# Performance work log

Measured on AMD Instinct MI355X. Metric: run time of the kernel, lower is better.

Reference implementation:

```python
import jax, jax.numpy as jnp
import numpy as np

DIM = 768
HEADS = 12
HEAD_DIM = DIM // HEADS
SEQ = 196
BATCH = 64
SCALE = HEAD_DIM ** -0.5


def setup_inputs() -> dict:
    key = jax.random.key(0)
    ks = jax.random.split(key, 5)
    x = jax.random.normal(ks[0], (BATCH, SEQ, DIM), dtype=jnp.float32)
    W_qkv = jax.random.normal(ks[1], (DIM, 3 * DIM), dtype=jnp.float32) * (DIM ** -0.5)
    static_a = jax.random.truncated_normal(ks[2], -2.0, 2.0, (1, HEADS, SEQ, SEQ), dtype=jnp.float32)
    W_proj = jax.random.normal(ks[3], (DIM, DIM), dtype=jnp.float32) * (DIM ** -0.5)
    b_proj = jnp.zeros((DIM,), dtype=jnp.float32)
    return {"x": x, "W_qkv": W_qkv, "static_a": static_a, "W_proj": W_proj, "b_proj": b_proj}


def reference(x, W_qkv, static_a, W_proj, b_proj):
    B, N, C = x.shape
    qkv = (x @ W_qkv).reshape(B, N, 3, HEADS, HEAD_DIM)
    qkv = jnp.transpose(qkv, (2, 0, 3, 1, 4))  # [3, B, H, N, D]
    q, k, v = qkv[0], qkv[1], qkv[2]
    attn = jnp.einsum('bhnd,bhmd->bhnm', q, k) * SCALE
    attn = jax.nn.softmax(attn, axis=-1) + static_a  # post-softmax additive bias
    out = jnp.einsum('bhnm,bhmd->bhnd', attn, v)  # [B, H, N, D]
    out = jnp.transpose(out, (0, 2, 1, 3)).reshape(B, N, C)
    return out @ W_proj + b_proj
```

## Files before the change

### kernel.cpp

```cpp
#include <hip/hip_runtime.h>
#include <stdint.h>

#define DIM 768
#define HEADS 12
#define SEQ 196
#define BATCH 64
#define NTOK (BATCH*SEQ)
#define QKVLD (3*DIM)
#define SCALE 0.125f

using short8  = __attribute__((ext_vector_type(8))) short;
using short4v = __attribute__((ext_vector_type(4))) short;
using float4v = __attribute__((ext_vector_type(4))) float;
using ushort4v = __attribute__((ext_vector_type(4))) unsigned short;

static __device__ __forceinline__ unsigned short f2bf(float f) {
  union { float f; unsigned u; } v; v.f = f;
  unsigned u = v.u;
  u += 0x7fffu + ((u >> 16) & 1u);
  return (unsigned short)(u >> 16);
}

#if defined(__has_builtin)
#if __has_builtin(__builtin_amdgcn_global_load_lds)
#define HAS_GLL 1
#endif
#endif

static __device__ __forceinline__ void gll16(const unsigned short* g, unsigned short* l) {
#ifdef HAS_GLL
  __builtin_amdgcn_global_load_lds(
      (const __attribute__((address_space(1))) void*)g,
      (__attribute__((address_space(3))) void*)l, 16, 0, 0);
#else
  const int lane = threadIdx.x & 63;
  *(short8*)(l + lane * 8) = *(const short8*)g;
#endif
}

__global__ __launch_bounds__(256) void cast_x_kernel(const float* __restrict__ in,
                                                     unsigned short* __restrict__ out) {
  int i = blockIdx.x * 256 + threadIdx.x;
  float4 v = ((const float4*)in)[i];
  ushort4v o;
  o.x = f2bf(v.x); o.y = f2bf(v.y); o.z = f2bf(v.z); o.w = f2bf(v.w);
  ((ushort4v*)out)[i] = o;
}

__global__ __launch_bounds__(256) void transpose_cast_kernel(const float* __restrict__ in,
                                                             unsigned short* __restrict__ out,
                                                             int R, int C) {
  __shared__ float tile[32][33];
  int c0 = blockIdx.x * 32, r0 = blockIdx.y * 32;
  int tx = threadIdx.x, ty = threadIdx.y;
  for (int i = 0; i < 32; i += 8)
    tile[ty + i][tx] = in[(size_t)(r0 + ty + i) * C + c0 + tx];
  __syncthreads();
  for (int i = 0; i < 32; i += 8)
    out[(size_t)(c0 + ty + i) * R + r0 + tx] = f2bf(tile[tx][ty + i]);
}

template <int MODE>
__global__ __launch_bounds__(256) void gemm_kernel(const unsigned short* __restrict__ A,
                                                   const unsigned short* __restrict__ Bt,
                                                   const float* __restrict__ bias,
                                                   unsigned short* __restrict__ outB,
                                                   float* __restrict__ outF) {
  constexpr int K = 768;
  __shared__ __align__(16) unsigned short Als[2][128 * 32];
  __shared__ __align__(16) unsigned short Bls[2][128 * 32];
  const int tid = threadIdx.x;
  const int wid = tid >> 6, lane = tid & 63;
  const int s = lane & 15, q = lane >> 4;
  const int wr = wid >> 1, wc = wid & 1;
  const int m0 = blockIdx.y * 128;
  const int n0 = blockIdx.x * 128;

  float4v acc[4][4];
  for (int i = 0; i < 4; i++)
    for (int j = 0; j < 4; j++) acc[i][j] = (float4v){0.f, 0.f, 0.f, 0.f};

  const int srow = lane >> 2;
  const int scol = (lane & 3) * 8;

  const unsigned short* ga = A  + (size_t)(m0 + wid * 32 + srow) * K + scol;
  const unsigned short* gb = Bt + (size_t)(n0 + wid * 32 + srow) * K + scol;
  unsigned short* la0 = &Als[0][wid * 32 * 32];
  unsigned short* la1 = &Als[1][wid * 32 * 32];
  unsigned short* lb0 = &Bls[0][wid * 32 * 32];
  unsigned short* lb1 = &Bls[1][wid * 32 * 32];

  for (int kt = 0; kt < K; kt += 64) {
    gll16(ga,                la0);
    gll16(ga + 16 * K,       la0 + 16 * 32);
    gll16(ga + 32,           la1);
    gll16(ga + 32 + 16 * K,  la1 + 16 * 32);
    gll16(gb,                lb0);
    gll16(gb + 16 * K,       lb0 + 16 * 32);
    gll16(gb + 32,           lb1);
    gll16(gb + 32 + 16 * K,  lb1 + 16 * 32);
    ga += 64; gb += 64;
    __syncthreads();

    for (int hh = 0; hh < 2; hh++) {
      short8 af[4], bfr[4];
      for (int i = 0; i < 4; i++)
        af[i] = *(const short8*)&Als[hh][(wr * 64 + i * 16 + s) * 32 + q * 8];
      for (int j = 0; j < 4; j++)
        bfr[j] = *(const short8*)&Bls[hh][(wc * 64 + j * 16 + s) * 32 + q * 8];
      for (int i = 0; i < 4; i++)
        for (int j = 0; j < 4; j++)
          acc[i][j] = __builtin_amdgcn_mfma_f32_16x16x32_bf16(bfr[j], af[i], acc[i][j], 0, 0, 0);
    }
    __syncthreads();
  }

  if (MODE == 0) {
    for (int i = 0; i < 4; i++) {
      size_t mrow = (size_t)(m0 + wr * 64 + i * 16 + s) * QKVLD;
      for (int j = 0; j < 4; j++) {
        int n = n0 + wc * 64 + j * 16 + q * 4;
        ushort4v ov;
        ov.x = f2bf(acc[i][j][0]); ov.y = f2bf(acc[i][j][1]);
        ov.z = f2bf(acc[i][j][2]); ov.w = f2bf(acc[i][j][3]);
        *(ushort4v*)&outB[mrow + n] = ov;
      }
    }
  } else {
    for (int i = 0; i < 4; i++) {
      size_t mrow = (size_t)(m0 + wr * 64 + i * 16 + s) * 768;
      for (int j = 0; j < 4; j++) {
        int n = n0 + wc * 64 + j * 16 + q * 4;
        float4v bv = *(const float4v*)&bias[n];
        float4v o;
        for (int r = 0; r < 4; r++) o[r] = acc[i][j][r] + bv[r];
        *(float4v*)&outF[mrow + n] = o;
      }
    }
  }
}

__global__ __launch_bounds__(256) void attn_kernel(const unsigned short* __restrict__ qkv,
                                                   const float* __restrict__ static_a,
                                                   unsigned short* __restrict__ outA) {
  constexpr int WV = 228;
  __shared__ __align__(16) unsigned short Vt[64 * WV];
  const int tid = threadIdx.x, wid = tid >> 6, lane = tid & 63;
  const int s = lane & 15, q = lane >> 4;
  const int bh = blockIdx.x;
  const int b = bh / 12, h = bh % 12;
  const unsigned short* Qb = qkv + (size_t)b * SEQ * QKVLD + h * 64;
  const unsigned short* Kb = Qb + 768;
  const unsigned short* Vb = Qb + 1536;

  {
    const int ms = tid & 63;
    const int d0 = (tid >> 6) * 16;
    for (int mb = 0; mb < 4; ++mb) {
      int m = mb * 64 + ms;
      if (m < 224) {
        if (m < 196) {
          short8 v0 = *(const short8*)&Vb[(size_t)m * QKVLD + d0];
          short8 v1 = *(const short8*)&Vb[(size_t)m * QKVLD + d0 + 8];
          for (int j = 0; j < 8; j++) Vt[(d0 + j) * WV + m] = (unsigned short)v0[j];
          for (int j = 0; j < 8; j++) Vt[(d0 + 8 + j) * WV + m] = (unsigned short)v1[j];
        } else {
          for (int j = 0; j < 16; j++) Vt[(d0 + j) * WV + m] = 0;
        }
      }
    }
  }
  __syncthreads();

  const int pmbase = (s >> 2) * 8 + (s & 3);

  for (int qt = wid; qt < 13; qt += 4) {
    const int n0 = qt * 16;
    const int nq = n0 + s;
    const int nql = nq > 195 ? 195 : nq;
    short8 qf0 = *(const short8*)&Qb[(size_t)nql * QKVLD + q * 8];
    short8 qf1 = *(const short8*)&Qb[(size_t)nql * QKVLD + 32 + q * 8];

    float4v sacc[14];
    for (int tt = 0; tt < 13; tt++) {
      int t = tt >> 1, h4 = tt & 1;
      int m = t * 32 + h4 * 4 + pmbase;
      if (m > 195) m = 195;
      short8 kf0 = *(const short8*)&Kb[(size_t)m * QKVLD + q * 8];
      short8 kf1 = *(const short8*)&Kb[(size_t)m * QKVLD + 32 + q * 8];
      float4v z = (float4v){0.f, 0.f, 0.f, 0.f};
      z = __builtin_amdgcn_mfma_f32_16x16x32_bf16(kf0, qf0, z, 0, 0, 0);
      z = __builtin_amdgcn_mfma_f32_16x16x32_bf16(kf1, qf1, z, 0, 0, 0);
      sacc[tt] = z;
    }
    sacc[13] = (float4v){0.f, 0.f, 0.f, 0.f};

    float mx = -3.0e38f;
    for (int tt = 0; tt < 12; tt++)
      for (int i = 0; i < 4; i++) mx = fmaxf(mx, sacc[tt][i]);
    if (q == 0)
      for (int i = 0; i < 4; i++) mx = fmaxf(mx, sacc[12][i]);
    mx = fmaxf(mx, __shfl_xor(mx, 16));
    mx = fmaxf(mx, __shfl_xor(mx, 32));
    const float CE = SCALE * 1.44269504f;
    float sm = 0.f;
    for (int tt = 0; tt < 12; tt++)
      for (int i = 0; i < 4; i++) {
        float e = __builtin_amdgcn_exp2f((sacc[tt][i] - mx) * CE);
        sacc[tt][i] = e; sm += e;
      }
    if (q == 0) {
      for (int i = 0; i < 4; i++) {
        float e = __builtin_amdgcn_exp2f((sacc[12][i] - mx) * CE);
        sacc[12][i] = e; sm += e;
      }
    } else {
      sacc[12] = (float4v){0.f, 0.f, 0.f, 0.f};
    }
    sm += __shfl_xor(sm, 16);
    sm += __shfl_xor(sm, 32);
    const float inv = 1.0f / sm;

    const float* sa = static_a + ((size_t)h * SEQ + nql) * SEQ;
    short8 pfrag[7];
    for (int t = 0; t < 7; t++) {
      short8 pf;
      for (int h4 = 0; h4 < 2; h4++) {
        int tt = 2 * t + h4;
        bool valid = (tt < 12) || (tt == 12 && q == 0);
        float4v a4 = (float4v){0.f, 0.f, 0.f, 0.f};
        if (valid) a4 = *(const float4v*)(sa + t * 32 + q * 8 + h4 * 4);
        int src = valid ? tt : 13;
        for (int i = 0; i < 4; i++) {
          float pv = valid ? (sacc[src][i] * inv + a4[i]) : 0.f;
          pf[h4 * 4 + i] = (short)f2bf(pv);
        }
      }
      pfrag[t] = pf;
    }

    for (int dt = 0; dt < 4; dt++) {
      float4v o = (float4v){0.f, 0.f, 0.f, 0.f};
      for (int t = 0; t < 7; t++) {
        const unsigned short* vp = &Vt[(dt * 16 + s) * WV + t * 32 + q * 8];
        short4v v0 = *(const short4v*)vp;
        short4v v1 = *(const short4v*)(vp + 4);
        short8 vf;
        vf[0] = v0[0]; vf[1] = v0[1]; vf[2] = v0[2]; vf[3] = v0[3];
        vf[4] = v1[0]; vf[5] = v1[1]; vf[6] = v1[2]; vf[7] = v1[3];
        o = __builtin_amdgcn_mfma_f32_16x16x32_bf16(vf, pfrag[t], o, 0, 0, 0);
      }
      if (nq < 196) {
        ushort4v ov;
        ov.x = f2bf(o[0]); ov.y = f2bf(o[1]); ov.z = f2bf(o[2]); ov.w = f2bf(o[3]);
        *(ushort4v*)&outA[((size_t)b * SEQ + nq) * DIM + h * 64 + dt * 16 + q * 4] = ov;
      }
    }
  }
}

extern "C" void kernel_launch(void* const* d_in, const int* in_sizes, int n_in,
                              void* d_out, int out_size, void* d_ws, size_t ws_size,
                              hipStream_t stream) {
  const float* x        = (const float*)d_in[0];
  const float* Wqkv     = (const float*)d_in[1];
  const float* static_a = (const float*)d_in[2];
  const float* Wproj    = (const float*)d_in[3];
  const float* bproj    = (const float*)d_in[4];
  float* out = (float*)d_out;

  unsigned char* ws = (unsigned char*)d_ws;
  size_t off = 0;
  unsigned short* qkv_ws = (unsigned short*)(ws + off); off += (size_t)NTOK * QKVLD * 2;
  unsigned short* xa_ws  = (unsigned short*)(ws + off); off += (size_t)NTOK * DIM * 2;
  unsigned short* wqkvt  = (unsigned short*)(ws + off); off += (size_t)3 * DIM * DIM * 2;
  unsigned short* wprojt = (unsigned short*)(ws + off); off += (size_t)DIM * DIM * 2;

  cast_x_kernel<<<NTOK * DIM / 4 / 256, 256, 0, stream>>>(x, xa_ws);
  transpose_cast_kernel<<<dim3(3 * DIM / 32, DIM / 32), dim3(32, 8), 0, stream>>>(Wqkv, wqkvt, DIM, 3 * DIM);
  transpose_cast_kernel<<<dim3(DIM / 32, DIM / 32), dim3(32, 8), 0, stream>>>(Wproj, wprojt, DIM, DIM);
  gemm_kernel<0><<<dim3(3 * DIM / 128, NTOK / 128), 256, 0, stream>>>(xa_ws, wqkvt, nullptr, qkv_ws, nullptr);
  attn_kernel<<<BATCH * HEADS, 256, 0, stream>>>(qkv_ws, static_a, xa_ws);
  gemm_kernel<1><<<dim3(DIM / 128, NTOK / 128), 256, 0, stream>>>(xa_ws, wprojt, bproj, nullptr, out);
}
```

Measured before the change: 263.8 us.

## Replace LDS-staged GEMM with per-wave register-tiled direct global loads

Both GEMMs drop shared-memory staging and block-wide barriers. Each wave now computes its own 64x64 output tile, loading MFMA fragments straight from global memory into double-buffered registers, and the launch becomes a 1D grid with an occupancy hint. This removes LDS traffic and __syncthreads stalls, but the four waves in a block no longer share loaded A/B tiles, so global/L2 traffic per FLOP rises and the fragment loads are strided 16-byte reads.

Result: slower. 395.8 us (+50.0%).

```diff
diff --git a/kernel.cpp b/kernel.cpp
--- a/kernel.cpp
+++ b/kernel.cpp
@@ -19,23 +19,6 @@
   unsigned u = v.u;
   u += 0x7fffu + ((u >> 16) & 1u);
   return (unsigned short)(u >> 16);
-}
-
-#if defined(__has_builtin)
-#if __has_builtin(__builtin_amdgcn_global_load_lds)
-#define HAS_GLL 1
-#endif
-#endif
-
-static __device__ __forceinline__ void gll16(const unsigned short* g, unsigned short* l) {
-#ifdef HAS_GLL
-  __builtin_amdgcn_global_load_lds(
-      (const __attribute__((address_space(1))) void*)g,
-      (__attribute__((address_space(3))) void*)l, 16, 0, 0);
-#else
-  const int lane = threadIdx.x & 63;
-  *(short8*)(l + lane * 8) = *(const short8*)g;
-#endif
 }
 
 __global__ __launch_bounds__(256) void cast_x_kernel(const float* __restrict__ in,
@@ -61,65 +44,56 @@
 }
 
 template <int MODE>
-__global__ __launch_bounds__(256) void gemm_kernel(const unsigned short* __restrict__ A,
-                                                   const unsigned short* __restrict__ Bt,
-                                                   const float* __restrict__ bias,
-                                                   unsigned short* __restrict__ outB,
-                                                   float* __restrict__ outF) {
+__global__ __launch_bounds__(256, 3) void gemm_kernel(const unsigned short* __restrict__ A,
+                                                      const unsigned short* __restrict__ Bt,
+                                                      const float* __restrict__ bias,
+                                                      unsigned short* __restrict__ outB,
+                                                      float* __restrict__ outF) {
   constexpr int K = 768;
-  __shared__ __align__(16) unsigned short Als[2][128 * 32];
-  __shared__ __align__(16) unsigned short Bls[2][128 * 32];
+  constexpr int NW = (MODE == 0 ? 2304 : 768) / 64;
   const int tid = threadIdx.x;
   const int wid = tid >> 6, lane = tid & 63;
   const int s = lane & 15, q = lane >> 4;
-  const int wr = wid >> 1, wc = wid & 1;
-  const int m0 = blockIdx.y * 128;
-  const int n0 = blockIdx.x * 128;
+
+  const int gw = blockIdx.x * 4 + wid;
+  const int mw = gw / NW, nw = gw % NW;
+  const int m0 = mw * 64, n0 = nw * 64;
+
+  const unsigned short* Ab = A  + (size_t)m0 * K + q * 8;
+  const unsigned short* Bb = Bt + (size_t)n0 * K + q * 8;
 
   float4v acc[4][4];
   for (int i = 0; i < 4; i++)
     for (int j = 0; j < 4; j++) acc[i][j] = (float4v){0.f, 0.f, 0.f, 0.f};
 
-  const int srow = lane >> 2;
-  const int scol = (lane & 3) * 8;
-
-  const unsigned short* ga = A  + (size_t)(m0 + wid * 32 + srow) * K + scol;
-  const unsigned short* gb = Bt + (size_t)(n0 + wid * 32 + srow) * K + scol;
-  unsigned short* la0 = &Als[0][wid * 32 * 32];
-  unsigned short* la1 = &Als[1][wid * 32 * 32];
-  unsigned short* lb0 = &Bls[0][wid * 32 * 32];
-  unsigned short* lb1 = &Bls[1][wid * 32 * 32];
-
-  for (int kt = 0; kt < K; kt += 64) {
-    gll16(ga,                la0);
-    gll16(ga + 16 * K,       la0 + 16 * 32);
-    gll16(ga + 32,           la1);
-    gll16(ga + 32 + 16 * K,  la1 + 16 * 32);
-    gll16(gb,                lb0);
-    gll16(gb + 16 * K,       lb0 + 16 * 32);
-    gll16(gb + 32,           lb1);
-    gll16(gb + 32 + 16 * K,  lb1 + 16 * 32);
-    ga += 64; gb += 64;
-    __syncthreads();
-
-    for (int hh = 0; hh < 2; hh++) {
-      short8 af[4], bfr[4];
-      for (int i = 0; i < 4; i++)
-        af[i] = *(const short8*)&Als[hh][(wr * 64 + i * 16 + s) * 32 + q * 8];
+  short8 af[2][4], bf[2][4];
+#pragma unroll
+  for (int i = 0; i < 4; i++) {
+    af[0][i] = *(const short8*)&Ab[(size_t)(i * 16 + s) * K];
+    bf[0][i] = *(const short8*)&Bb[(size_t)(i * 16 + s) * K];
+  }
+#pragma unroll
+  for (int kt = 0; kt < K; kt += 32) {
+    const int pb = (kt >> 5) & 1;
+    if (kt + 32 < K) {
+#pragma unroll
+      for (int i = 0; i < 4; i++) {
+        af[pb ^ 1][i] = *(const short8*)&Ab[(size_t)(i * 16 + s) * K + kt + 32];
+        bf[pb ^ 1][i] = *(const short8*)&Bb[(size_t)(i * 16 + s) * K + kt + 32];
+      }
+    }
+#pragma unroll
+    for (int i = 0; i < 4; i++)
+#pragma unroll
       for (int j = 0; j < 4; j++)
-        bfr[j] = *(const short8*)&Bls[hh][(wc * 64 + j * 16 + s) * 32 + q * 8];
-      for (int i = 0; i < 4; i++)
-        for (int j = 0; j < 4; j++)
-          acc[i][j] = __builtin_amdgcn_mfma_f32_16x16x32_bf16(bfr[j], af[i], acc[i][j], 0, 0, 0);
-    }
-    __syncthreads();
+        acc[i][j] = __builtin_amdgcn_mfma_f32_16x16x32_bf16(bf[pb][j], af[pb][i], acc[i][j], 0, 0, 0);
   }
 
   if (MODE == 0) {
     for (int i = 0; i < 4; i++) {
-      size_t mrow = (size_t)(m0 + wr * 64 + i * 16 + s) * QKVLD;
+      size_t mrow = (size_t)(m0 + i * 16 + s) * QKVLD;
       for (int j = 0; j < 4; j++) {
-        int n = n0 + wc * 64 + j * 16 + q * 4;
+        int n = n0 + j * 16 + q * 4;
         ushort4v ov;
         ov.x = f2bf(acc[i][j][0]); ov.y = f2bf(acc[i][j][1]);
         ov.z = f2bf(acc[i][j][2]); ov.w = f2bf(acc[i][j][3]);
@@ -128,9 +102,9 @@
     }
   } else {
     for (int i = 0; i < 4; i++) {
-      size_t mrow = (size_t)(m0 + wr * 64 + i * 16 + s) * 768;
+      size_t mrow = (size_t)(m0 + i * 16 + s) * 768;
       for (int j = 0; j < 4; j++) {
-        int n = n0 + wc * 64 + j * 16 + q * 4;
+        int n = n0 + j * 16 + q * 4;
         float4v bv = *(const float4v*)&bias[n];
         float4v o;
         for (int r = 0; r < 4; r++) o[r] = acc[i][j][r] + bv[r];
@@ -279,7 +253,7 @@
   cast_x_kernel<<<NTOK * DIM / 4 / 256, 256, 0, stream>>>(x, xa_ws);
   transpose_cast_kernel<<<dim3(3 * DIM / 32, DIM / 32), dim3(32, 8), 0, stream>>>(Wqkv, wqkvt, DIM, 3 * DIM);
   transpose_cast_kernel<<<dim3(DIM / 32, DIM / 32), dim3(32, 8), 0, stream>>>(Wproj, wprojt, DIM, DIM);
-  gemm_kernel<0><<<dim3(3 * DIM / 128, NTOK / 128), 256, 0, stream>>>(xa_ws, wqkvt, nullptr, qkv_ws, nullptr);
+  gemm_kernel<0><<<196 * 36 / 4, 256, 0, stream>>>(xa_ws, wqkvt, nullptr, qkv_ws, nullptr);
   attn_kernel<<<BATCH * HEADS, 256, 0, stream>>>(qkv_ws, static_a, xa_ws);
-  gemm_kernel<1><<<dim3(DIM / 128, NTOK / 128), 256, 0, stream>>>(xa_ws, wprojt, bproj, nullptr, out);
-}
+  gemm_kernel<1><<<196 * 12 / 4, 256, 0, stream>>>(xa_ws, wprojt, bproj, nullptr, out);
+}
```

## Merge cast/transpose prepasses into one launch and shrink GEMM tiles to 128x64

Applied to the files above, without the earlier changes.

Combines the x cast and both weight transpose-casts into a single prepass kernel, cutting two launches. The GEMM tile shrinks from 128x128 with a K-step of 64 to 128x64 with a K-step of 32. LDS use and accumulator count drop, and launch_bounds requests 5 blocks per SM for higher occupancy. In exchange, each block reuses its loaded data less and issues twice as many barriers per K.

Result: slower. 269.9 us (+2.3%).

```diff
diff --git a/kernel.cpp b/kernel.cpp
--- a/kernel.cpp
+++ b/kernel.cpp
@@ -38,88 +38,96 @@
 #endif
 }
 
-__global__ __launch_bounds__(256) void cast_x_kernel(const float* __restrict__ in,
-                                                     unsigned short* __restrict__ out) {
-  int i = blockIdx.x * 256 + threadIdx.x;
-  float4 v = ((const float4*)in)[i];
-  ushort4v o;
-  o.x = f2bf(v.x); o.y = f2bf(v.y); o.z = f2bf(v.z); o.w = f2bf(v.w);
-  ((ushort4v*)out)[i] = o;
-}
-
-__global__ __launch_bounds__(256) void transpose_cast_kernel(const float* __restrict__ in,
-                                                             unsigned short* __restrict__ out,
-                                                             int R, int C) {
+__global__ __launch_bounds__(256) void prepass_kernel(const float* __restrict__ x,
+                                                      const float* __restrict__ Wqkv,
+                                                      const float* __restrict__ Wproj,
+                                                      unsigned short* __restrict__ xbf,
+                                                      unsigned short* __restrict__ wqkvt,
+                                                      unsigned short* __restrict__ wprojt) {
+  const int bid = blockIdx.x, tid = threadIdx.x;
+  if (bid < 9408) {
+    int i = bid * 256 + tid;
+    float4 v = ((const float4*)x)[i];
+    ushort4v o;
+    o.x = f2bf(v.x); o.y = f2bf(v.y); o.z = f2bf(v.z); o.w = f2bf(v.w);
+    ((ushort4v*)xbf)[i] = o;
+    return;
+  }
   __shared__ float tile[32][33];
-  int c0 = blockIdx.x * 32, r0 = blockIdx.y * 32;
-  int tx = threadIdx.x, ty = threadIdx.y;
+  const float* src; unsigned short* dst; int C, b;
+  if (bid < 11136) { src = Wqkv; dst = wqkvt; C = 2304; b = bid - 9408; }
+  else             { src = Wproj; dst = wprojt; C = 768;  b = bid - 11136; }
+  const int R = 768;
+  const int ntx = C / 32;
+  const int c0 = (b % ntx) * 32, r0 = (b / ntx) * 32;
+  const int tx = tid & 31, ty = tid >> 5;
   for (int i = 0; i < 32; i += 8)
-    tile[ty + i][tx] = in[(size_t)(r0 + ty + i) * C + c0 + tx];
+    tile[ty + i][tx] = src[(size_t)(r0 + ty + i) * C + c0 + tx];
   __syncthreads();
   for (int i = 0; i < 32; i += 8)
-    out[(size_t)(c0 + ty + i) * R + r0 + tx] = f2bf(tile[tx][ty + i]);
+    dst[(size_t)(c0 + ty + i) * R + r0 + tx] = f2bf(tile[tx][ty + i]);
 }
 
 template <int MODE>
-__global__ __launch_bounds__(256) void gemm_kernel(const unsigned short* __restrict__ A,
-                                                   const unsigned short* __restrict__ Bt,
-                                                   const float* __restrict__ bias,
-                                                   unsigned short* __restrict__ outB,
-                                                   float* __restrict__ outF) {
+__global__ __launch_bounds__(256, 5) void gemm_kernel(const unsigned short* __restrict__ A,
+                                                      const unsigned short* __restrict__ Bt,
+                                                      const float* __restrict__ bias,
+                                                      unsigned short* __restrict__ outB,
+                                                      float* __restrict__ outF) {
   constexpr int K = 768;
-  __shared__ __align__(16) unsigned short Als[2][128 * 32];
-  __shared__ __align__(16) unsigned short Bls[2][128 * 32];
+  __shared__ __align__(16) unsigned short Als[128 * 32];
+  __shared__ __align__(16) unsigned short Bls[64 * 32];
   const int tid = threadIdx.x;
   const int wid = tid >> 6, lane = tid & 63;
   const int s = lane & 15, q = lane >> 4;
   const int wr = wid >> 1, wc = wid & 1;
   const int m0 = blockIdx.y * 128;
-  const int n0 = blockIdx.x * 128;
-
-  float4v acc[4][4];
+  const int n0 = blockIdx.x * 64;
+
+  float4v acc[4][2];
+#pragma unroll
   for (int i = 0; i < 4; i++)
-    for (int j = 0; j < 4; j++) acc[i][j] = (float4v){0.f, 0.f, 0.f, 0.f};
+#pragma unroll
+    for (int j = 0; j < 2; j++) acc[i][j] = (float4v){0.f, 0.f, 0.f, 0.f};
 
   const int srow = lane >> 2;
   const int scol = (lane & 3) * 8;
 
   const unsigned short* ga = A  + (size_t)(m0 + wid * 32 + srow) * K + scol;
-  const unsigned short* gb = Bt + (size_t)(n0 + wid * 32 + srow) * K + scol;
-  unsigned short* la0 = &Als[0][wid * 32 * 32];
-  unsigned short* la1 = &Als[1][wid * 32 * 32];
-  unsigned short* lb0 = &Bls[0][wid * 32 * 32];
-  unsigned short* lb1 = &Bls[1][wid * 32 * 32];
-
-  for (int kt = 0; kt < K; kt += 64) {
-    gll16(ga,                la0);
-    gll16(ga + 16 * K,       la0 + 16 * 32);
-    gll16(ga + 32,           la1);
-    gll16(ga + 32 + 16 * K,  la1 + 16 * 32);
-    gll16(gb,                lb0);
-    gll16(gb + 16 * K,       lb0 + 16 * 32);
-    gll16(gb + 32,           lb1);
-    gll16(gb + 32 + 16 * K,  lb1 + 16 * 32);
-    ga += 64; gb += 64;
+  const unsigned short* gb = Bt + (size_t)(n0 + wid * 16 + srow) * K + scol;
+  unsigned short* la = &Als[wid * 32 * 32];
+  unsigned short* lb = &Bls[wid * 16 * 32];
+
+#pragma unroll 2
+  for (int kt = 0; kt < K; kt += 32) {
+    gll16(ga,          la);
+    gll16(ga + 16 * K, la + 16 * 32);
+    gll16(gb,          lb);
+    ga += 32; gb += 32;
     __syncthreads();
 
-    for (int hh = 0; hh < 2; hh++) {
-      short8 af[4], bfr[4];
-      for (int i = 0; i < 4; i++)
-        af[i] = *(const short8*)&Als[hh][(wr * 64 + i * 16 + s) * 32 + q * 8];
-      for (int j = 0; j < 4; j++)
-        bfr[j] = *(const short8*)&Bls[hh][(wc * 64 + j * 16 + s) * 32 + q * 8];
-      for (int i = 0; i < 4; i++)
-        for (int j = 0; j < 4; j++)
-          acc[i][j] = __builtin_amdgcn_mfma_f32_16x16x32_bf16(bfr[j], af[i], acc[i][j], 0, 0, 0);
-    }
+    short8 af[4], bf[2];
+#pragma unroll
+    for (int i = 0; i < 4; i++)
+      af[i] = *(const short8*)&Als[(wr * 64 + i * 16 + s) * 32 + q * 8];
+#pragma unroll
+    for (int j = 0; j < 2; j++)
+      bf[j] = *(const short8*)&Bls[(wc * 32 + j * 16 + s) * 32 + q * 8];
+#pragma unroll
+    for (int i = 0; i < 4; i++)
+#pragma unroll
+      for (int j = 0; j < 2; j++)
+        acc[i][j] = __builtin_amdgcn_mfma_f32_16x16x32_bf16(bf[j], af[i], acc[i][j], 0, 0, 0);
     __syncthreads();
   }
 
   if (MODE == 0) {
+#pragma unroll
     for (int i = 0; i < 4; i++) {
       size_t mrow = (size_t)(m0 + wr * 64 + i * 16 + s) * QKVLD;
-      for (int j = 0; j < 4; j++) {
-        int n = n0 + wc * 64 + j * 16 + q * 4;
+#pragma unroll
+      for (int j = 0; j < 2; j++) {
+        int n = n0 + wc * 32 + j * 16 + q * 4;
         ushort4v ov;
         ov.x = f2bf(acc[i][j][0]); ov.y = f2bf(acc[i][j][1]);
         ov.z = f2bf(acc[i][j][2]); ov.w = f2bf(acc[i][j][3]);
@@ -127,10 +135,12 @@
       }
     }
   } else {
+#pragma unroll
     for (int i = 0; i < 4; i++) {
       size_t mrow = (size_t)(m0 + wr * 64 + i * 16 + s) * 768;
-      for (int j = 0; j < 4; j++) {
-        int n = n0 + wc * 64 + j * 16 + q * 4;
+#pragma unroll
+      for (int j = 0; j < 2; j++) {
+        int n = n0 + wc * 32 + j * 16 + q * 4;
         float4v bv = *(const float4v*)&bias[n];
         float4v o;
         for (int r = 0; r < 4; r++) o[r] = acc[i][j][r] + bv[r];
@@ -276,10 +286,8 @@
   unsigned short* wqkvt  = (unsigned short*)(ws + off); off += (size_t)3 * DIM * DIM * 2;
   unsigned short* wprojt = (unsigned short*)(ws + off); off += (size_t)DIM * DIM * 2;
 
-  cast_x_kernel<<<NTOK * DIM / 4 / 256, 256, 0, stream>>>(x, xa_ws);
-  transpose_cast_kernel<<<dim3(3 * DIM / 32, DIM / 32), dim3(32, 8), 0, stream>>>(Wqkv, wqkvt, DIM, 3 * DIM);
-  transpose_cast_kernel<<<dim3(DIM / 32, DIM / 32), dim3(32, 8), 0, stream>>>(Wproj, wprojt, DIM, DIM);
-  gemm_kernel<0><<<dim3(3 * DIM / 128, NTOK / 128), 256, 0, stream>>>(xa_ws, wqkvt, nullptr, qkv_ws, nullptr);
+  prepass_kernel<<<11712, 256, 0, stream>>>(x, Wqkv, Wproj, xa_ws, wqkvt, wprojt);
+  gemm_kernel<0><<<dim3(2304 / 64, NTOK / 128), 256, 0, stream>>>(xa_ws, wqkvt, nullptr, qkv_ws, nullptr);
   attn_kernel<<<BATCH * HEADS, 256, 0, stream>>>(qkv_ws, static_a, xa_ws);
-  gemm_kernel<1><<<dim3(DIM / 128, NTOK / 128), 256, 0, stream>>>(xa_ws, wprojt, bproj, nullptr, out);
-}
+  gemm_kernel<1><<<dim3(768 / 64, NTOK / 128), 256, 0, stream>>>(xa_ws, wprojt, bproj, nullptr, out);
+}
```
